# Kernel optimization log

Measured on AMD Instinct MI355X. Metric: run time of the kernel, lower is better.

The kernel has to match this reference:

```python
import jax, jax.numpy as jnp
import numpy as np

# static sizes
B = 32          # graphs
NPER = 1024     # nodes per graph
N0 = B * NPER
F_IN = 128
H = 4           # heads
DH = 32         # per-head dim (128/4)
HID = H * DH    # 128
E = 524288      # edges (avg degree 16)
K1, K2, K3 = 512, 256, 128  # ceil(0.5*nper) per stage
NC = 10


def gcn_agg(h, src, dst, w, n):
    """GCNConv propagation: sym-normalized aggregation with self-loops.
    h: [n,F] already projected; w: [E] edge weight (0 for filtered edges)."""
    deg = jax.ops.segment_sum(w, dst, num_segments=n) + 1.0  # +1 self-loop
    dinv = jax.lax.rsqrt(deg)
    coef = dinv[src] * dinv[dst] * w                          # [E]
    agg = jax.ops.segment_sum(h[src] * coef[:, None], dst, num_segments=n)
    return agg + h / deg[:, None]  # self-loop term: dinv[i]^2 = 1/deg[i]


def mh_gcn(x, W, b, src, dst, w, n):
    """MAGPoolGCNLayer: per-head GCNConv (32->32), relu, concat heads."""
    h = jnp.einsum('nhd,hde->nhe', x.reshape(n, H, DH), W).reshape(n, HID)
    return jax.nn.relu(gcn_agg(h, src, dst, w, n) + b.reshape(HID))


def att_pool(x, src, dst, w, A, psW, psb, n, k):
    """MultiHeadAtt: standard att, complex score, concat pooling, global weight."""
    sub = x.reshape(n, H, DH)
    att = jnp.einsum('nhd,hd->nh', sub, A)            # per-head Linear(32,1)
    cat = (att[:, :, None] * sub).reshape(n, HID)     # score*sub, concat
    score = (gcn_agg(cat @ psW, src, dst, w, n) + psb)[:, 0]  # GCNConv(HID,1)
    nper = n // B
    _, idx = jax.lax.top_k(score.reshape(B, nper), k)  # per-graph topk
    perm = (idx + jnp.arange(B)[:, None] * nper).reshape(-1)
    xn = x[perm] * jnp.tanh(score[perm])[:, None]      # global att weighting
    # filter_adj: remap kept nodes, mask edges touching dropped nodes
    nmap = jnp.full((n,), -1, jnp.int32).at[perm].set(jnp.arange(B * k, dtype=jnp.int32))
    ns, nd = nmap[src], nmap[dst]
    wn = w * ((ns >= 0) & (nd >= 0)).astype(w.dtype)
    return xn, jnp.maximum(ns, 0), jnp.maximum(nd, 0), wn


def readout(x):
    # graphs are contiguous with equal node counts -> reshape readout
    xr = x.reshape(B, -1, x.shape[-1])
    return jnp.concatenate([xr.max(1), xr.mean(1)], axis=1)  # [B, 2*HID]


def setup_inputs():
    key = jax.random.key(0)
    ks = jax.random.split(key, 26)
    gid = jnp.repeat(jnp.arange(B, dtype=jnp.int32), E // B)
    src = jax.random.randint(ks[0], (E,), 0, NPER, dtype=jnp.int32) + gid * NPER
    dst = jax.random.randint(ks[1], (E,), 0, NPER, dtype=jnp.int32) + gid * NPER
    x = jax.random.normal(ks[2], (N0, F_IN), jnp.float32)
    s = 0.1
    def rn(k, shp):
        return jax.random.normal(k, shp, jnp.float32) * s
    return {
        'x': x, 'src': src, 'dst': dst,
        'W1': rn(ks[3], (H, DH, DH)), 'b1': rn(ks[4], (H, DH)), 'A1': rn(ks[5], (H, DH)),
        'ps1W': rn(ks[6], (HID, 1)), 'ps1b': rn(ks[7], (1,)),
        'W2': rn(ks[8], (H, DH, DH)), 'b2': rn(ks[9], (H, DH)), 'A2': rn(ks[10], (H, DH)),
        'ps2W': rn(ks[11], (HID, 1)), 'ps2b': rn(ks[12], (1,)),
        'W3': rn(ks[13], (H, DH, DH)), 'b3': rn(ks[14], (H, DH)), 'A3': rn(ks[15], (H, DH)),
        'ps3W': rn(ks[16], (HID, 1)), 'ps3b': rn(ks[17], (1,)),
        'l1W': rn(ks[18], (2 * HID, HID)), 'l1b': rn(ks[19], (HID,)),
        'l2W': rn(ks[20], (HID, HID // 2)), 'l2b': rn(ks[21], (HID // 2,)),
        'l3W': rn(ks[22], (HID // 2, NC)), 'l3b': rn(ks[23], (NC,)),
    }


def reference(x, src, dst, W1, b1, A1, ps1W, ps1b, W2, b2, A2, ps2W, ps2b,
              W3, b3, A3, ps3W, ps3b, l1W, l1b, l2W, l2b, l3W, l3b):
    w = jnp.ones((E,), x.dtype)
    h = mh_gcn(x, W1, b1, src, dst, w, N0)
    h, s1, d1, w1 = att_pool(h, src, dst, w, A1, ps1W, ps1b, N0, K1)
    r1 = readout(h)
    n1 = B * K1
    h = mh_gcn(h, W2, b2, s1, d1, w1, n1)
    h, s2, d2, w2 = att_pool(h, s1, d1, w1, A2, ps2W, ps2b, n1, K2)
    r2 = readout(h)
    n2 = B * K2
    h = mh_gcn(h, W3, b3, s2, d2, w2, n2)
    h, _, _, _ = att_pool(h, s2, d2, w2, A3, ps3W, ps3b, n2, K3)
    r3 = readout(h)
    z = r1 + r2 + r3                      # [B, 2*HID]
    z = jax.nn.relu(z @ l1W + l1b)        # dropout skipped (eval mode)
    z = jax.nn.relu(z @ l2W + l2b)
    return jax.nn.log_softmax(z @ l3W + l3b, axis=-1)
```

## Files before the change

kernel.cpp:

```cpp
#include <hip/hip_runtime.h>
#include <math.h>

#define BGR 32
#define NPER0 1024
#define N0 (BGR * NPER0)
#define FDIM 128
#define EDG 524288
#define K1 512
#define K2 256
#define K3 128
#define EBLK (EDG / 256)
#define EPG (EDG / BGR)
#define SXP 36
#define CAP 64

__device__ __forceinline__ unsigned enc_f(float v) {
    unsigned u = __float_as_uint(v);
    return (u & 0x80000000u) ? ~u : (u | 0x80000000u);
}
__device__ __forceinline__ float dec_f(unsigned u) {
    return (u & 0x80000000u) ? __uint_as_float(u ^ 0x80000000u) : __uint_as_float(~u);
}

__global__ void zero_all(int* __restrict__ cntA, unsigned* __restrict__ rmax,
                         float* __restrict__ rsum) {
    int i = blockIdx.x * 256 + threadIdx.x;
    if (i < N0) cntA[i] = 0;
    if (i < 2 * BGR * FDIM) { rmax[i] = 0u; rsum[i] = 0.0f; }
}

__device__ __forceinline__ void proj_compute(float* __restrict__ hp, int nb, int t,
                                             const float* __restrict__ sW,
                                             const float* __restrict__ sxT) {
    const int fg = t >> 3, ng = t & 7, h = fg >> 3;
    const float* ap = sxT + h * 32 * SXP + ng * 4;
    const float* bp = sW + h * 1024 + (fg & 7) * 4;
    float4 acc0 = {0.f, 0.f, 0.f, 0.f}, acc1 = acc0, acc2 = acc0, acc3 = acc0;
#pragma unroll
    for (int k = 0; k < 32; k++) {
        float4 a = *(const float4*)(ap + k * SXP);
        float4 b = *(const float4*)(bp + k * 32);
        acc0.x = fmaf(a.x, b.x, acc0.x); acc0.y = fmaf(a.x, b.y, acc0.y);
        acc0.z = fmaf(a.x, b.z, acc0.z); acc0.w = fmaf(a.x, b.w, acc0.w);
        acc1.x = fmaf(a.y, b.x, acc1.x); acc1.y = fmaf(a.y, b.y, acc1.y);
        acc1.z = fmaf(a.y, b.z, acc1.z); acc1.w = fmaf(a.y, b.w, acc1.w);
        acc2.x = fmaf(a.z, b.x, acc2.x); acc2.y = fmaf(a.z, b.y, acc2.y);
        acc2.z = fmaf(a.z, b.z, acc2.z); acc2.w = fmaf(a.z, b.w, acc2.w);
        acc3.x = fmaf(a.w, b.x, acc3.x); acc3.y = fmaf(a.w, b.y, acc3.y);
        acc3.z = fmaf(a.w, b.z, acc3.z); acc3.w = fmaf(a.w, b.w, acc3.w);
    }
    float4* op = (float4*)(hp + (size_t)(nb + ng * 4) * FDIM + fg * 4);
    op[0] = acc0; op[32] = acc1; op[64] = acc2; op[96] = acc3;
}

__device__ __forceinline__ void pool_body(const float* __restrict__ ha,
                                          const int* __restrict__ perm,
                                          const float* __restrict__ mult, int k, int pb,
                                          unsigned* __restrict__ rmax,
                                          float* __restrict__ rsum,
                                          float* __restrict__ smax,
                                          float* __restrict__ ssum) {
    const int t = threadIdx.x;
    const int g = pb & 31;
    const int c = pb >> 5;
    const int f = t & 127, half = t >> 7;
    const int base = g * k + c * 32;
    float vmax = -1e30f, vsum = 0.0f;
#pragma unroll
    for (int j0 = 0; j0 < 16; j0++) {
        int newid = base + half + j0 * 2;
        int old = perm[newid];
        float m = mult[newid];
        float v = ha[(size_t)old * FDIM + f] * m;
        vmax = fmaxf(vmax, v);
        vsum += v;
    }
    if (half) { smax[f] = vmax; ssum[f] = vsum; }
    __syncthreads();
    if (!half) {
        vmax = fmaxf(vmax, smax[f]);
        vsum += ssum[f];
        atomicMax(&rmax[g * FDIM + f], enc_f(vmax));
        atomicAdd(&rsum[g * FDIM + f], vsum);
    }
}

__global__ void bin_proj1(const int* __restrict__ src, const int* __restrict__ dst,
                          int* __restrict__ cnt, int* __restrict__ slot,
                          const float* __restrict__ x, const float* __restrict__ W,
                          float* __restrict__ hp) {
    __shared__ __align__(16) float sW[4096];
    __shared__ __align__(16) float sxT[128 * SXP];
    const int t = threadIdx.x;
    if (blockIdx.x < EBLK) {
        const int g = blockIdx.x & 31, chunk = blockIdx.x >> 5;
        int e = g * EPG + chunk * 256 + t;
        int s = src[e];
        int d = dst[e];
        int p = atomicAdd(&cnt[d], 1);
        if (p < CAP) slot[d * CAP + p] = s;
        return;
    }
    const int tb = blockIdx.x - EBLK;
    const int nb = (tb & 31) * NPER0 + (tb >> 5) * 32;
    for (int i = t; i < 4096; i += 256) sW[i] = W[i];
    for (int i = t; i < 4096; i += 256) {
        int node = i >> 7, dim = i & 127;
        sxT[dim * SXP + node] = x[(size_t)(nb + node) * FDIM + dim];
    }
    __syncthreads();
    proj_compute(hp, nb, t, sW, sxT);
}

__global__ void bin_proj_pool(const int* __restrict__ cnt_prev,
                              const int* __restrict__ slot_prev,
                              const int* __restrict__ nmap,
                              int* __restrict__ cnt_next, int* __restrict__ slot_next,
                              const float* __restrict__ ha, const int* __restrict__ perm,
                              const float* __restrict__ mult, const float* __restrict__ W,
                              float* __restrict__ hp, int ncomp, int ntiles, int kprev,
                              unsigned* __restrict__ rmax, float* __restrict__ rsum) {
    __shared__ __align__(16) float sW[4096];
    __shared__ __align__(16) float sxT[128 * SXP];
    const int t = threadIdx.x;
    if (blockIdx.x < ncomp) {
        const int w = t >> 6, lane = t & 63;
        const int b = (blockIdx.x & 31) * kprev + (blockIdx.x >> 5) * 4 + w;
        const int old = perm[b];
        const int c = min(cnt_prev[old], CAP);
        int a = -1;
        if (lane < c) a = nmap[slot_prev[(size_t)old * CAP + lane]];
        unsigned long long mk = __ballot(a >= 0);
        if (a >= 0) {
            int pos = __popcll(mk & ((1ull << lane) - 1ull));
            slot_next[(size_t)b * CAP + pos] = a;
        }
        if (lane == 0) cnt_next[b] = __popcll(mk);
        return;
    }
    if (blockIdx.x >= ncomp + ntiles) {
        pool_body(ha, perm, mult, kprev, blockIdx.x - (ncomp + ntiles), rmax, rsum,
                  sW, sW + 128);
        return;
    }
    const int tb = blockIdx.x - ncomp;
    const int nb = (tb & 31) * kprev + (tb >> 5) * 32;
    for (int i = t; i < 4096; i += 256) sW[i] = W[i];
    for (int i = t; i < 4096; i += 256) {
        int node = i >> 7, dim = i & 127;
        int newid = nb + node;
        sxT[dim * SXP + node] = ha[(size_t)perm[newid] * FDIM + dim] * mult[newid];
    }
    __syncthreads();
    proj_compute(hp, nb, t, sW, sxT);
}

__global__ void agg_kernel(const float* __restrict__ hp, const float* __restrict__ b,
                           const int* __restrict__ cnt, const int* __restrict__ slot,
                           const float* __restrict__ A, const float* __restrict__ psW,
                           float* __restrict__ ha, float* __restrict__ csd, int nper) {
    const int w = threadIdx.x >> 6;
    const int lane = threadIdx.x & 63;
    const int g = blockIdx.x & 31;
    const int chunk = blockIdx.x >> 5;
    const int i = g * nper + chunk * 4 + w;
    const int ci = cnt[i];
    const float di = rsqrtf((float)ci + 1.0f);
    const int c = min(ci, CAP);
    const float2* __restrict__ hp2 = (const float2*)hp;
    float2 self = hp2[(size_t)i * 64 + lane];
    float accx = self.x * di * di, accy = self.y * di * di;
    int idx = 0;
    float dv = 0.0f;
    if (lane < c) {
        idx = slot[i * CAP + lane];
        dv = rsqrtf((float)cnt[idx] + 1.0f);
    }
    int j = 0;
    for (; j + 3 < c; j += 4) {
        int s0 = __shfl(idx, j, 64);
        int s1 = __shfl(idx, j + 1, 64);
        int s2 = __shfl(idx, j + 2, 64);
        int s3 = __shfl(idx, j + 3, 64);
        float c0 = __shfl(dv, j, 64) * di;
        float c1 = __shfl(dv, j + 1, 64) * di;
        float c2 = __shfl(dv, j + 2, 64) * di;
        float c3 = __shfl(dv, j + 3, 64) * di;
        float2 v0 = hp2[(size_t)s0 * 64 + lane];
        float2 v1 = hp2[(size_t)s1 * 64 + lane];
        float2 v2 = hp2[(size_t)s2 * 64 + lane];
        float2 v3 = hp2[(size_t)s3 * 64 + lane];
        accx = fmaf(v0.x, c0, accx); accy = fmaf(v0.y, c0, accy);
        accx = fmaf(v1.x, c1, accx); accy = fmaf(v1.y, c1, accy);
        accx = fmaf(v2.x, c2, accx); accy = fmaf(v2.y, c2, accy);
        accx = fmaf(v3.x, c3, accx); accy = fmaf(v3.y, c3, accy);
    }
    for (; j < c; j++) {
        int s = __shfl(idx, j, 64);
        float co = __shfl(dv, j, 64) * di;
        float2 v = hp2[(size_t)s * 64 + lane];
        accx = fmaf(v.x, co, accx); accy = fmaf(v.y, co, accy);
    }
    float2 bb = ((const float2*)b)[lane];
    float2 o;
    o.x = fmaxf(accx + bb.x, 0.0f);
    o.y = fmaxf(accy + bb.y, 0.0f);
    ((float2*)ha)[(size_t)i * 64 + lane] = o;
    float2 Av = ((const float2*)A)[lane];
    float2 Pv = ((const float2*)psW)[lane];
    float a = o.x * Av.x + o.y * Av.y;
    float p = o.x * Pv.x + o.y * Pv.y;
#pragma unroll
    for (int d = 8; d > 0; d >>= 1) {
        a += __shfl_down(a, d, 16);
        p += __shfl_down(p, d, 16);
    }
    float part = a * p;
    part += __shfl_down(part, 16, 64);
    part += __shfl_down(part, 32, 64);
    if (lane == 0) csd[i] = part * di;
}

__global__ void score_kernel(const float* __restrict__ csd, const int* __restrict__ cnt,
                             const int* __restrict__ slot, const float* __restrict__ psb,
                             float* __restrict__ scout, int nper) {
    const int w = threadIdx.x >> 6;
    const int lane = threadIdx.x & 63;
    const int g = blockIdx.x & 31;
    const int chunk = blockIdx.x >> 5;
    const int i = g * nper + chunk * 4 + w;
    const int ci = cnt[i];
    const int c = min(ci, CAP);
    float v = 0.0f;
    if (lane < c) v = csd[slot[(size_t)i * CAP + lane]];
#pragma unroll
    for (int d = 32; d > 0; d >>= 1) v += __shfl_xor(v, d, 64);
    if (lane == 0)
        scout[i] = rsqrtf((float)ci + 1.0f) * (v + csd[i]) + psb[0];
}

__global__ void topk_kernel(const float* __restrict__ scin, int nper, int k,
                            int* __restrict__ nmap, int* __restrict__ perm,
                            float* __restrict__ mult) {
    __shared__ float sc[NPER0];
    __shared__ unsigned ukey[NPER0];
    __shared__ unsigned hist[256];
    __shared__ unsigned wtot[4];
    __shared__ unsigned sel[2];
    __shared__ int ctr[2];
    const int g = blockIdx.x, t = threadIdx.x;
    const int w = t >> 6, l = t & 63;
    const int gnb = g * nper;
    for (int i = t; i < nper; i += 256) {
        float v = scin[gnb + i];
        sc[i] = v;
        ukey[i] = enc_f(v);
    }
    if (t == 0) { sel[0] = 0u; sel[1] = (unsigned)k; }
    __syncthreads();
    for (int shift = 24; shift >= 0; shift -= 8) {
        hist[t] = 0u;
        __syncthreads();
        const unsigned prefix = sel[0];
        const unsigned need = sel[1];
        for (int i = t; i < nper; i += 256) {
            unsigned u = ukey[i];
            bool inp = (shift == 24) || ((u >> (shift + 8)) == (prefix >> (shift + 8)));
            int dig = inp ? (int)((u >> shift) & 255u) : -1;
            int cv = inp ? 1 : 0;
#pragma unroll
            for (int d = 1; d < 64; d <<= 1) {
                int od = __shfl_xor(dig, d, 64);
                int oc = __shfl_xor(cv, d, 64);
                if (od == dig) cv = ((l & d) == 0) ? (cv + oc) : 0;
            }
            if (dig >= 0 && cv > 0) atomicAdd(&hist[dig], (unsigned)cv);
        }
        __syncthreads();
        const unsigned h = hist[t];
        unsigned s = h;
#pragma unroll
        for (int off = 1; off < 64; off <<= 1) {
            unsigned v = __shfl_down(s, off, 64);
            if (l + off < 64) s += v;
        }
        if (l == 0) wtot[w] = s;
        __syncthreads();
        unsigned add = 0;
        for (int ww = w + 1; ww < 4; ww++) add += wtot[ww];
        const unsigned sfx = s + add;
        const unsigned gtr = sfx - h;
        if (sfx >= need && gtr < need) {
            sel[0] = prefix | ((unsigned)t << shift);
            sel[1] = need - gtr;
        }
        __syncthreads();
    }
    const unsigned T = sel[0];
    const int need = (int)sel[1];
    if (t == 0) { ctr[0] = 0; ctr[1] = k - need; }
    __syncthreads();
    for (int i = t; i < nper; i += 256) {
        unsigned u = ukey[i];
        int node = gnb + i;
        int newid = -1;
        if (u > T) {
            newid = g * k + atomicAdd(&ctr[0], 1);
        } else if (u == T) {
            int slot2 = atomicAdd(&ctr[1], 1);
            if (slot2 < k) newid = g * k + slot2;
        }
        nmap[node] = newid;
        if (newid >= 0) {
            perm[newid] = node;
            mult[newid] = tanhf(sc[i]);
        }
    }
}

__global__ void final_mlp(const float* __restrict__ ha, const int* __restrict__ perm,
                          const float* __restrict__ mult,
                          const unsigned* __restrict__ rmax, const float* __restrict__ rsum,
                          const float* __restrict__ l1W, const float* __restrict__ l1b,
                          const float* __restrict__ l2W, const float* __restrict__ l2b,
                          const float* __restrict__ l3W, const float* __restrict__ l3b,
                          float* __restrict__ out) {
    __shared__ float sz[256], s1[128], s2[64], s3[10], red[2], sm2[128], ss2[128];
    const int g = blockIdx.x, t = threadIdx.x;
    const int RS = BGR * FDIM;
    const int f = t & 127, half = t >> 7;
    float vmax = -1e30f, vsum = 0.0f;
#pragma unroll 8
    for (int j0 = 0; j0 < 64; j0++) {
        int newid = g * K3 + half + j0 * 2;
        int old = perm[newid];
        float m = mult[newid];
        float v = ha[(size_t)old * FDIM + f] * m;
        vmax = fmaxf(vmax, v);
        vsum += v;
    }
    if (half) { sm2[f] = vmax; ss2[f] = vsum; }
    __syncthreads();
    if (!half) {
        vmax = fmaxf(vmax, sm2[f]);
        vsum += ss2[f];
        sz[f] = dec_f(rmax[g * FDIM + f]) + dec_f(rmax[RS + g * FDIM + f]) + vmax;
        sz[f + 128] = rsum[g * FDIM + f] / (float)K1 + rsum[RS + g * FDIM + f] / (float)K2 +
                      vsum / (float)K3;
    }
    __syncthreads();
    if (t < 128) {
        float acc = l1b[t];
        for (int i = 0; i < 256; i++) acc = fmaf(sz[i], l1W[i * 128 + t], acc);
        s1[t] = fmaxf(acc, 0.0f);
    }
    __syncthreads();
    if (t < 64) {
        float a2 = l2b[t];
        for (int i = 0; i < 128; i++) a2 = fmaf(s1[i], l2W[i * 64 + t], a2);
        s2[t] = fmaxf(a2, 0.0f);
    }
    __syncthreads();
    if (t < 10) {
        float a3 = l3b[t];
        for (int i = 0; i < 64; i++) a3 = fmaf(s2[i], l3W[i * 10 + t], a3);
        s3[t] = a3;
    }
    __syncthreads();
    if (t == 0) {
        float m = -1e30f;
        for (int c = 0; c < 10; c++) m = fmaxf(m, s3[c]);
        float sum = 0.0f;
        for (int c = 0; c < 10; c++) sum += expf(s3[c] - m);
        red[0] = m;
        red[1] = logf(sum);
    }
    __syncthreads();
    if (t < 10) out[g * 10 + t] = s3[t] - red[0] - red[1];
}

extern "C" void kernel_launch(void* const* d_in, const int* in_sizes, int n_in,
                              void* d_out, int out_size, void* d_ws, size_t ws_size,
                              hipStream_t stream) {
    const float* x    = (const float*)d_in[0];
    const int* src0   = (const int*)d_in[1];
    const int* dst0   = (const int*)d_in[2];
    const float* W1   = (const float*)d_in[3];
    const float* b1   = (const float*)d_in[4];
    const float* A1   = (const float*)d_in[5];
    const float* ps1W = (const float*)d_in[6];
    const float* ps1b = (const float*)d_in[7];
    const float* W2   = (const float*)d_in[8];
    const float* b2   = (const float*)d_in[9];
    const float* A2   = (const float*)d_in[10];
    const float* ps2W = (const float*)d_in[11];
    const float* ps2b = (const float*)d_in[12];
    const float* W3   = (const float*)d_in[13];
    const float* b3   = (const float*)d_in[14];
    const float* A3   = (const float*)d_in[15];
    const float* ps3W = (const float*)d_in[16];
    const float* ps3b = (const float*)d_in[17];
    const float* l1W  = (const float*)d_in[18];
    const float* l1b  = (const float*)d_in[19];
    const float* l2W  = (const float*)d_in[20];
    const float* l2b  = (const float*)d_in[21];
    const float* l3W  = (const float*)d_in[22];
    const float* l3b  = (const float*)d_in[23];
    float* out = (float*)d_out;

    char* ws = (char*)d_ws;
    size_t o = 0;
    auto alloc = [&](size_t bytes) -> void* {
        void* p = ws + o;
        o += (bytes + 255) & ~(size_t)255;
        return p;
    };
    float*    hproj = (float*)alloc((size_t)N0 * FDIM * 4);
    float*    hact  = (float*)alloc((size_t)N0 * FDIM * 4);
    int*      cntA  = (int*)alloc(N0 * 4);
    int*      cntB  = (int*)alloc(BGR * K1 * 4);
    int*      cntC  = (int*)alloc(BGR * K2 * 4);
    int*      slotA = (int*)alloc((size_t)N0 * CAP * 4);
    int*      slotB = (int*)alloc((size_t)BGR * K1 * CAP * 4);
    int*      slotC = (int*)alloc((size_t)BGR * K2 * CAP * 4);
    float*    cs    = (float*)alloc(N0 * 4);
    float*    scb   = (float*)alloc(N0 * 4);
    int*      nmapA = (int*)alloc(N0 * 4);
    int*      nmapB = (int*)alloc(BGR * K1 * 4);
    int*      nmapC = (int*)alloc(BGR * K2 * 4);
    int*      perm  = (int*)alloc(BGR * K1 * 4);
    float*    mult  = (float*)alloc(BGR * K1 * 4);
    unsigned* rmax  = (unsigned*)alloc(2 * BGR * FDIM * 4);
    float*    rsum  = (float*)alloc(2 * BGR * FDIM * 4);

    const int n1 = BGR * K1, n2 = BGR * K2;
    const int RS = BGR * FDIM;

    zero_all<<<N0 / 256, 256, 0, stream>>>(cntA, rmax, rsum);
    bin_proj1<<<EBLK + N0 / 32, 256, 0, stream>>>(src0, dst0, cntA, slotA, x, W1, hproj);
    agg_kernel<<<N0 / 4, 256, 0, stream>>>(hproj, b1, cntA, slotA, A1, ps1W, hact, cs, NPER0);
    score_kernel<<<N0 / 4, 256, 0, stream>>>(cs, cntA, slotA, ps1b, scb, NPER0);
    topk_kernel<<<BGR, 256, 0, stream>>>(scb, NPER0, K1, nmapA, perm, mult);

    bin_proj_pool<<<n1 / 4 + n1 / 32 + BGR * K1 / 32, 256, 0, stream>>>(
        cntA, slotA, nmapA, cntB, slotB, hact, perm, mult, W2, hproj,
        n1 / 4, n1 / 32, K1, rmax, rsum);
    agg_kernel<<<n1 / 4, 256, 0, stream>>>(hproj, b2, cntB, slotB, A2, ps2W, hact, cs, K1);
    score_kernel<<<n1 / 4, 256, 0, stream>>>(cs, cntB, slotB, ps2b, scb, K1);
    topk_kernel<<<BGR, 256, 0, stream>>>(scb, K1, K2, nmapB, perm, mult);

    bin_proj_pool<<<n2 / 4 + n2 / 32 + BGR * K2 / 32, 256, 0, stream>>>(
        cntB, slotB, nmapB, cntC, slotC, hact, perm, mult, W3, hproj,
        n2 / 4, n2 / 32, K2, rmax + RS, rsum + RS);
    agg_kernel<<<n2 / 4, 256, 0, stream>>>(hproj, b3, cntC, slotC, A3, ps3W, hact, cs, K2);
    score_kernel<<<n2 / 4, 256, 0, stream>>>(cs, cntC, slotC, ps3b, scb, K2);
    topk_kernel<<<BGR, 256, 0, stream>>>(scb, K2, K3, nmapC, perm, mult);

    final_mlp<<<BGR, 256, 0, stream>>>(hact, perm, mult, rmax, rsum,
                                       l1W, l1b, l2W, l2b, l3W, l3b, out);

    (void)in_sizes; (void)n_in; (void)out_size; (void)ws_size;
}
```

Baseline: 260.2 us.

## Fuse score into topk, per-graph LDS edge binning, widen pooling kernels

Removes the zero_all and score_kernel launches. Edge binning now runs in one block per graph using LDS counters, and that block also zeroes the readout buffers. Score aggregation moves into a 1024-thread topk kernel that reads csd from shared memory. The pool blocks handle 8 nodes instead of 32 to raise parallelism, and the final MLP uses 1024 threads for the stage-3 readout. The trade-off is that binning now runs on only 32 blocks, serialising global slot writes, and the score neighbor loop runs per thread instead of per wavefront.

```diff
diff --git a/kernel.cpp b/kernel.cpp
--- a/kernel.cpp
+++ b/kernel.cpp
@@ -6,13 +6,15 @@
 #define N0 (BGR * NPER0)
 #define FDIM 128
 #define EDG 524288
+#define EPG (EDG / BGR)
 #define K1 512
 #define K2 256
 #define K3 128
-#define EBLK (EDG / 256)
-#define EPG (EDG / BGR)
+#define N1 (BGR * K1)
+#define N2 (BGR * K2)
 #define SXP 36
 #define CAP 64
+#define RSEC (BGR * FDIM)
 
 __device__ __forceinline__ unsigned enc_f(float v) {
     unsigned u = __float_as_uint(v);
@@ -20,13 +22,6 @@
 }
 __device__ __forceinline__ float dec_f(unsigned u) {
     return (u & 0x80000000u) ? __uint_as_float(u ^ 0x80000000u) : __uint_as_float(~u);
-}
-
-__global__ void zero_all(int* __restrict__ cntA, unsigned* __restrict__ rmax,
-                         float* __restrict__ rsum) {
-    int i = blockIdx.x * 256 + threadIdx.x;
-    if (i < N0) cntA[i] = 0;
-    if (i < 2 * BGR * FDIM) { rmax[i] = 0u; rsum[i] = 0.0f; }
 }
 
 __device__ __forceinline__ void proj_compute(float* __restrict__ hp, int nb, int t,
@@ -64,10 +59,10 @@
     const int g = pb & 31;
     const int c = pb >> 5;
     const int f = t & 127, half = t >> 7;
-    const int base = g * k + c * 32;
+    const int base = g * k + c * 8;
     float vmax = -1e30f, vsum = 0.0f;
 #pragma unroll
-    for (int j0 = 0; j0 < 16; j0++) {
+    for (int j0 = 0; j0 < 4; j0++) {
         int newid = base + half + j0 * 2;
         int old = perm[newid];
         float m = mult[newid];
@@ -88,20 +83,34 @@
 __global__ void bin_proj1(const int* __restrict__ src, const int* __restrict__ dst,
                           int* __restrict__ cnt, int* __restrict__ slot,
                           const float* __restrict__ x, const float* __restrict__ W,
-                          float* __restrict__ hp) {
+                          float* __restrict__ hp,
+                          unsigned* __restrict__ rmax, float* __restrict__ rsum) {
     __shared__ __align__(16) float sW[4096];
     __shared__ __align__(16) float sxT[128 * SXP];
     const int t = threadIdx.x;
-    if (blockIdx.x < EBLK) {
-        const int g = blockIdx.x & 31, chunk = blockIdx.x >> 5;
-        int e = g * EPG + chunk * 256 + t;
-        int s = src[e];
-        int d = dst[e];
-        int p = atomicAdd(&cnt[d], 1);
-        if (p < CAP) slot[d * CAP + p] = s;
+    if (blockIdx.x < BGR) {
+        const int g = blockIdx.x;
+        int* lcnt = (int*)sW;
+        for (int i = t; i < NPER0; i += 256) lcnt[i] = 0;
+        {
+            int z = g * 256 + t;
+            rmax[z] = 0u;
+            rsum[z] = 0.0f;
+        }
+        __syncthreads();
+        const int eb = g * EPG;
+        for (int r = 0; r < EPG / 256; r++) {
+            int e = eb + r * 256 + t;
+            int s = src[e];
+            int d = dst[e];
+            int p = atomicAdd(&lcnt[d - g * NPER0], 1);
+            if (p < CAP) slot[(size_t)d * CAP + p] = s;
+        }
+        __syncthreads();
+        for (int i = t; i < NPER0; i += 256) cnt[g * NPER0 + i] = lcnt[i];
         return;
     }
-    const int tb = blockIdx.x - EBLK;
+    const int tb = blockIdx.x - BGR;
     const int nb = (tb & 31) * NPER0 + (tb >> 5) * 32;
     for (int i = t; i < 4096; i += 256) sW[i] = W[i];
     for (int i = t; i < 4096; i += 256) {
@@ -112,14 +121,14 @@
     proj_compute(hp, nb, t, sW, sxT);
 }
 
-__global__ void bin_proj_pool(const int* __restrict__ cnt_prev,
-                              const int* __restrict__ slot_prev,
-                              const int* __restrict__ nmap,
-                              int* __restrict__ cnt_next, int* __restrict__ slot_next,
-                              const float* __restrict__ ha, const int* __restrict__ perm,
-                              const float* __restrict__ mult, const float* __restrict__ W,
-                              float* __restrict__ hp, int ncomp, int ntiles, int kprev,
-                              unsigned* __restrict__ rmax, float* __restrict__ rsum) {
+__global__ void comp_proj_pool(const int* __restrict__ cnt_prev,
+                               const int* __restrict__ slot_prev,
+                               const int* __restrict__ nmap,
+                               int* __restrict__ cnt_next, int* __restrict__ slot_next,
+                               const float* __restrict__ ha, const int* __restrict__ perm,
+                               const float* __restrict__ mult, const float* __restrict__ W,
+                               float* __restrict__ hp, int ncomp, int ntiles, int kprev,
+                               unsigned* __restrict__ rmax, float* __restrict__ rsum) {
     __shared__ __align__(16) float sW[4096];
     __shared__ __align__(16) float sxT[128 * SXP];
     const int t = threadIdx.x;
@@ -221,27 +230,12 @@
     if (lane == 0) csd[i] = part * di;
 }
 
-__global__ void score_kernel(const float* __restrict__ csd, const int* __restrict__ cnt,
-                             const int* __restrict__ slot, const float* __restrict__ psb,
-                             float* __restrict__ scout, int nper) {
-    const int w = threadIdx.x >> 6;
-    const int lane = threadIdx.x & 63;
-    const int g = blockIdx.x & 31;
-    const int chunk = blockIdx.x >> 5;
-    const int i = g * nper + chunk * 4 + w;
-    const int ci = cnt[i];
-    const int c = min(ci, CAP);
-    float v = 0.0f;
-    if (lane < c) v = csd[slot[(size_t)i * CAP + lane]];
-#pragma unroll
-    for (int d = 32; d > 0; d >>= 1) v += __shfl_xor(v, d, 64);
-    if (lane == 0)
-        scout[i] = rsqrtf((float)ci + 1.0f) * (v + csd[i]) + psb[0];
-}
-
-__global__ void topk_kernel(const float* __restrict__ scin, int nper, int k,
-                            int* __restrict__ nmap, int* __restrict__ perm,
-                            float* __restrict__ mult) {
+__global__ __launch_bounds__(1024) void topk_kernel(
+        const float* __restrict__ csd, const int* __restrict__ cnt,
+        const int* __restrict__ slot, const float* __restrict__ psb,
+        int nper, int k, int* __restrict__ nmap, int* __restrict__ perm,
+        float* __restrict__ mult) {
+    __shared__ float cs_l[NPER0];
     __shared__ float sc[NPER0];
     __shared__ unsigned ukey[NPER0];
     __shared__ unsigned hist[256];
@@ -249,23 +243,31 @@
     __shared__ unsigned sel[2];
     __shared__ int ctr[2];
     const int g = blockIdx.x, t = threadIdx.x;
-    const int w = t >> 6, l = t & 63;
     const int gnb = g * nper;
-    for (int i = t; i < nper; i += 256) {
-        float v = scin[gnb + i];
-        sc[i] = v;
-        ukey[i] = enc_f(v);
-    }
+    if (t < nper) cs_l[t] = csd[gnb + t];
     if (t == 0) { sel[0] = 0u; sel[1] = (unsigned)k; }
     __syncthreads();
+    if (t < nper) {
+        int ci = cnt[gnb + t];
+        int c = min(ci, CAP);
+        const int* srow = slot + (size_t)(gnb + t) * CAP;
+        float v = 0.0f;
+        for (int j = 0; j < c; j++) v += cs_l[srow[j] - gnb];
+        float s = rsqrtf((float)ci + 1.0f) * (v + cs_l[t]) + psb[0];
+        sc[t] = s;
+        ukey[t] = enc_f(s);
+    }
+    __syncthreads();
+    const int w4 = t >> 6, l = t & 63;
     for (int shift = 24; shift >= 0; shift -= 8) {
-        hist[t] = 0u;
+        if (t < 256) hist[t] = 0u;
         __syncthreads();
         const unsigned prefix = sel[0];
         const unsigned need = sel[1];
-        for (int i = t; i < nper; i += 256) {
-            unsigned u = ukey[i];
-            bool inp = (shift == 24) || ((u >> (shift + 8)) == (prefix >> (shift + 8)));
+        {
+            unsigned u = (t < nper) ? ukey[t] : 0u;
+            bool inp = (t < nper) &&
+                       ((shift == 24) || ((u >> (shift + 8)) == (prefix >> (shift + 8))));
             int dig = inp ? (int)((u >> shift) & 255u) : -1;
             int cv = inp ? 1 : 0;
 #pragma unroll
@@ -277,76 +279,88 @@
             if (dig >= 0 && cv > 0) atomicAdd(&hist[dig], (unsigned)cv);
         }
         __syncthreads();
-        const unsigned h = hist[t];
-        unsigned s = h;
-#pragma unroll
-        for (int off = 1; off < 64; off <<= 1) {
-            unsigned v = __shfl_down(s, off, 64);
-            if (l + off < 64) s += v;
-        }
-        if (l == 0) wtot[w] = s;
-        __syncthreads();
-        unsigned add = 0;
-        for (int ww = w + 1; ww < 4; ww++) add += wtot[ww];
-        const unsigned sfx = s + add;
-        const unsigned gtr = sfx - h;
-        if (sfx >= need && gtr < need) {
-            sel[0] = prefix | ((unsigned)t << shift);
-            sel[1] = need - gtr;
+        unsigned h = 0, s = 0;
+        if (t < 256) {
+            h = hist[t];
+            s = h;
+#pragma unroll
+            for (int off = 1; off < 64; off <<= 1) {
+                unsigned v2 = __shfl_down(s, off, 64);
+                if (l + off < 64) s += v2;
+            }
+            if (l == 0) wtot[w4] = s;
+        }
+        __syncthreads();
+        if (t < 256) {
+            unsigned add = 0;
+            for (int ww = w4 + 1; ww < 4; ww++) add += wtot[ww];
+            const unsigned sfx = s + add;
+            const unsigned gtr = sfx - h;
+            if (sfx >= need && gtr < need) {
+                sel[0] = prefix | ((unsigned)t << shift);
+                sel[1] = need - gtr;
+            }
         }
         __syncthreads();
     }
     const unsigned T = sel[0];
-    const int need = (int)sel[1];
-    if (t == 0) { ctr[0] = 0; ctr[1] = k - need; }
-    __syncthreads();
-    for (int i = t; i < nper; i += 256) {
-        unsigned u = ukey[i];
-        int node = gnb + i;
+    const int need2 = (int)sel[1];
+    if (t == 0) { ctr[0] = 0; ctr[1] = k - need2; }
+    __syncthreads();
+    if (t < nper) {
+        unsigned u = ukey[t];
         int newid = -1;
         if (u > T) {
-            newid = g * k + atomicAdd(&ctr[0], 1);
+            newid = atomicAdd(&ctr[0], 1);
         } else if (u == T) {
-            int slot2 = atomicAdd(&ctr[1], 1);
-            if (slot2 < k) newid = g * k + slot2;
-        }
-        nmap[node] = newid;
+            int s2 = atomicAdd(&ctr[1], 1);
+            if (s2 < k) newid = s2;
+        }
+        nmap[gnb + t] = (newid >= 0) ? g * k + newid : -1;
         if (newid >= 0) {
-            perm[newid] = node;
-            mult[newid] = tanhf(sc[i]);
-        }
-    }
-}
-
-__global__ void final_mlp(const float* __restrict__ ha, const int* __restrict__ perm,
-                          const float* __restrict__ mult,
-                          const unsigned* __restrict__ rmax, const float* __restrict__ rsum,
-                          const float* __restrict__ l1W, const float* __restrict__ l1b,
-                          const float* __restrict__ l2W, const float* __restrict__ l2b,
-                          const float* __restrict__ l3W, const float* __restrict__ l3b,
-                          float* __restrict__ out) {
-    __shared__ float sz[256], s1[128], s2[64], s3[10], red[2], sm2[128], ss2[128];
+            perm[g * k + newid] = gnb + t;
+            mult[g * k + newid] = tanhf(sc[t]);
+        }
+    }
+}
+
+__global__ __launch_bounds__(1024) void pool3_mlp(
+        const float* __restrict__ ha, const int* __restrict__ perm,
+        const float* __restrict__ mult,
+        const unsigned* __restrict__ rmax, const float* __restrict__ rsum,
+        const float* __restrict__ l1W, const float* __restrict__ l1b,
+        const float* __restrict__ l2W, const float* __restrict__ l2b,
+        const float* __restrict__ l3W, const float* __restrict__ l3b,
+        float* __restrict__ out) {
+    __shared__ float pm[8][FDIM], ps[8][FDIM];
+    __shared__ float sz[256], s1[128], s2[64], s3[16], red[2];
     const int g = blockIdx.x, t = threadIdx.x;
-    const int RS = BGR * FDIM;
-    const int f = t & 127, half = t >> 7;
+    const int f = t & 127, ch = t >> 7;
     float vmax = -1e30f, vsum = 0.0f;
-#pragma unroll 8
-    for (int j0 = 0; j0 < 64; j0++) {
-        int newid = g * K3 + half + j0 * 2;
-        int old = perm[newid];
-        float m = mult[newid];
+#pragma unroll
+    for (int j = 0; j < K3 / 8; j++) {
+        int nid = g * K3 + ch + j * 8;
+        int old = perm[nid];
+        float m = mult[nid];
         float v = ha[(size_t)old * FDIM + f] * m;
         vmax = fmaxf(vmax, v);
         vsum += v;
     }
-    if (half) { sm2[f] = vmax; ss2[f] = vsum; }
-    __syncthreads();
-    if (!half) {
-        vmax = fmaxf(vmax, sm2[f]);
-        vsum += ss2[f];
-        sz[f] = dec_f(rmax[g * FDIM + f]) + dec_f(rmax[RS + g * FDIM + f]) + vmax;
-        sz[f + 128] = rsum[g * FDIM + f] / (float)K1 + rsum[RS + g * FDIM + f] / (float)K2 +
-                      vsum / (float)K3;
+    pm[ch][f] = vmax;
+    ps[ch][f] = vsum;
+    __syncthreads();
+    if (t < 128) {
+        float M = pm[0][t];
+#pragma unroll
+        for (int c2 = 1; c2 < 8; c2++) M = fmaxf(M, pm[c2][t]);
+        sz[t] = dec_f(rmax[g * FDIM + t]) + dec_f(rmax[RSEC + g * FDIM + t]) + M;
+    } else if (t < 256) {
+        int f2 = t - 128;
+        float S = ps[0][f2];
+#pragma unroll
+        for (int c2 = 1; c2 < 8; c2++) S += ps[c2][f2];
+        sz[t] = rsum[g * FDIM + f2] / (float)K1 + rsum[RSEC + g * FDIM + f2] / (float)K2 +
+                S / (float)K3;
     }
     __syncthreads();
     if (t < 128) {
@@ -418,46 +432,41 @@
     float*    hproj = (float*)alloc((size_t)N0 * FDIM * 4);
     float*    hact  = (float*)alloc((size_t)N0 * FDIM * 4);
     int*      cntA  = (int*)alloc(N0 * 4);
-    int*      cntB  = (int*)alloc(BGR * K1 * 4);
-    int*      cntC  = (int*)alloc(BGR * K2 * 4);
+    int*      cntB  = (int*)alloc(N1 * 4);
+    int*      cntC  = (int*)alloc(N2 * 4);
     int*      slotA = (int*)alloc((size_t)N0 * CAP * 4);
-    int*      slotB = (int*)alloc((size_t)BGR * K1 * CAP * 4);
-    int*      slotC = (int*)alloc((size_t)BGR * K2 * CAP * 4);
+    int*      slotB = (int*)alloc((size_t)N1 * CAP * 4);
+    int*      slotC = (int*)alloc((size_t)N2 * CAP * 4);
     float*    cs    = (float*)alloc(N0 * 4);
-    float*    scb   = (float*)alloc(N0 * 4);
     int*      nmapA = (int*)alloc(N0 * 4);
-    int*      nmapB = (int*)alloc(BGR * K1 * 4);
-    int*      nmapC = (int*)alloc(BGR * K2 * 4);
-    int*      perm  = (int*)alloc(BGR * K1 * 4);
-    float*    mult  = (float*)alloc(BGR * K1 * 4);
-    unsigned* rmax  = (unsigned*)alloc(2 * BGR * FDIM * 4);
-    float*    rsum  = (float*)alloc(2 * BGR * FDIM * 4);
-
-    const int n1 = BGR * K1, n2 = BGR * K2;
-    const int RS = BGR * FDIM;
-
-    zero_all<<<N0 / 256, 256, 0, stream>>>(cntA, rmax, rsum);
-    bin_proj1<<<EBLK + N0 / 32, 256, 0, stream>>>(src0, dst0, cntA, slotA, x, W1, hproj);
+    int*      nmapB = (int*)alloc(N1 * 4);
+    int*      perm  = (int*)alloc(N1 * 4);
+    float*    mult  = (float*)alloc(N1 * 4);
+    unsigned* rmax  = (unsigned*)alloc(2 * RSEC * 4);
+    float*    rsum  = (float*)alloc(2 * RSEC * 4);
+
+    bin_proj1<<<BGR + N0 / 32, 256, 0, stream>>>(src0, dst0, cntA, slotA, x, W1,
+                                                 hproj, rmax, rsum);
     agg_kernel<<<N0 / 4, 256, 0, stream>>>(hproj, b1, cntA, slotA, A1, ps1W, hact, cs, NPER0);
-    score_kernel<<<N0 / 4, 256, 0, stream>>>(cs, cntA, slotA, ps1b, scb, NPER0);
-    topk_kernel<<<BGR, 256, 0, stream>>>(scb, NPER0, K1, nmapA, perm, mult);
-
-    bin_proj_pool<<<n1 / 4 + n1 / 32 + BGR * K1 / 32, 256, 0, stream>>>(
+    topk_kernel<<<BGR, 1024, 0, stream>>>(cs, cntA, slotA, ps1b, NPER0, K1,
+                                          nmapA, perm, mult);
+
+    comp_proj_pool<<<N1 / 4 + N1 / 32 + BGR * K1 / 8, 256, 0, stream>>>(
         cntA, slotA, nmapA, cntB, slotB, hact, perm, mult, W2, hproj,
-        n1 / 4, n1 / 32, K1, rmax, rsum);
-    agg_kernel<<<n1 / 4, 256, 0, stream>>>(hproj, b2, cntB, slotB, A2, ps2W, hact, cs, K1);
-    score_kernel<<<n1 / 4, 256, 0, stream>>>(cs, cntB, slotB, ps2b, scb, K1);
-    topk_kernel<<<BGR, 256, 0, stream>>>(scb, K1, K2, nmapB, perm, mult);
-
-    bin_proj_pool<<<n2 / 4 + n2 / 32 + BGR * K2 / 32, 256, 0, stream>>>(
+        N1 / 4, N1 / 32, K1, rmax, rsum);
+    agg_kernel<<<N1 / 4, 256, 0, stream>>>(hproj, b2, cntB, slotB, A2, ps2W, hact, cs, K1);
+    topk_kernel<<<BGR, 1024, 0, stream>>>(cs, cntB, slotB, ps2b, K1, K2,
+                                          nmapB, perm, mult);
+
+    comp_proj_pool<<<N2 / 4 + N2 / 32 + BGR * K2 / 8, 256, 0, stream>>>(
         cntB, slotB, nmapB, cntC, slotC, hact, perm, mult, W3, hproj,
-        n2 / 4, n2 / 32, K2, rmax + RS, rsum + RS);
-    agg_kernel<<<n2 / 4, 256, 0, stream>>>(hproj, b3, cntC, slotC, A3, ps3W, hact, cs, K2);
-    score_kernel<<<n2 / 4, 256, 0, stream>>>(cs, cntC, slotC, ps3b, scb, K2);
-    topk_kernel<<<BGR, 256, 0, stream>>>(scb, K2, K3, nmapC, perm, mult);
-
-    final_mlp<<<BGR, 256, 0, stream>>>(hact, perm, mult, rmax, rsum,
-                                       l1W, l1b, l2W, l2b, l3W, l3b, out);
+        N2 / 4, N2 / 32, K2, rmax + RSEC, rsum + RSEC);
+    agg_kernel<<<N2 / 4, 256, 0, stream>>>(hproj, b3, cntC, slotC, A3, ps3W, hact, cs, K2);
+    topk_kernel<<<BGR, 1024, 0, stream>>>(cs, cntC, slotC, ps3b, K2, K3,
+                                          nmapA , perm, mult);
+
+    pool3_mlp<<<BGR, 1024, 0, stream>>>(hact, perm, mult, rmax, rsum,
+                                        l1W, l1b, l2W, l2b, l3W, l3b, out);
 
     (void)in_sizes; (void)n_in; (void)out_size; (void)ws_size;
 }
```

After: 260.3 us. About the same (+0.0%).
